# Performance work log

Hardware: AMD Instinct MI355X
Metric: run time of the kernel (lower is better)

Reference implementation:

```python
import jax, jax.numpy as jnp
import numpy as np

C, H, W = 512, 192, 192  # feature map dims; 3x3 patches at stride 3 (non-overlapping)


def setup_inputs() -> dict:
    key = jax.random.key(0)
    k1, k2 = jax.random.split(key)
    model_resp = jax.random.normal(k1, (1, C, H, W), dtype=jnp.float32)
    style_resp = jax.random.normal(k2, (1, C, H, W), dtype=jnp.float32)
    return {"model_resp": model_resp, "style_resp": style_resp}


def _unfold3(x):
    # torch.nn.Unfold(kernel=3, stride=3) on (1, C, H, W) -> (C*9, L) after the
    # module's view(patch_count, patch_size) (note: rows are feature channels,
    # columns are spatial locations, matching the original code's dim order).
    _, c, h, w = x.shape
    p = x[0].reshape(c, h // 3, 3, w // 3, 3)          # (c, ph, kh, pw, kw)
    p = p.transpose(0, 2, 4, 1, 3)                      # (c, kh, kw, ph, pw)
    return p.reshape(c * 9, (h // 3) * (w // 3))        # (A, L)


def reference(model_resp, style_resp):
    img = _unfold3(model_resp)                          # (A, L)
    sty = _unfold3(style_resp)                          # (A, L)
    img_norm = 1.0 / jnp.linalg.norm(img, axis=1)       # (A,)
    sty_norm = 1.0 / jnp.linalg.norm(sty, axis=1)       # (A,)
    S = img @ sty.T                                     # (A, A), S[i,j] = img_i . sty_j
    # Faithful to torch: expand(A, A) of a 1-D tensor broadcasts along dim 0,
    # i.e. multiplies COLUMNS by the normalizer vector.
    S1 = S * img_norm[None, :]
    S2 = S1.T * sty_norm[None, :]                       # S2[i,j] = img_norm[i]*sty_norm[j]*(img_j . sty_i)
    nearest = jnp.argmax(S2, axis=0)                    # (A,) int
    max_sim = jnp.max(S2, axis=0)                       # (A,) float (the online-max values)
    return nearest, max_sim
```

## Files before the change

kernel.cpp:

```cpp
#include <hip/hip_runtime.h>
#include <hip/hip_bf16.h>
#include <hip/hip_fp16.h>

#define A_DIM 4608
#define L_DIM 4096
#define CH    512
#define H_DIM 192
#define W_DIM 192

#define BM 128
#define BN 128
#define BK 32
#define NS (L_DIM / BK)

#define CPB 32

typedef _Float16 half8 __attribute__((ext_vector_type(8)));
typedef float   floatx4 __attribute__((ext_vector_type(4)));
typedef float   floatx16 __attribute__((ext_vector_type(16)));

__global__ __launch_bounds__(256) void prep_kernel(
    const float* __restrict__ x0, const float* __restrict__ x1,
    _Float16* __restrict__ Uhi0, _Float16* __restrict__ Ulo0,
    _Float16* __restrict__ Uhi1, _Float16* __restrict__ Ulo1,
    float* __restrict__ ss0, float* __restrict__ ss1) {
  const int which = blockIdx.z;
  const float* __restrict__ x = which ? x1 : x0;
  _Float16* __restrict__ Uhi = which ? Uhi1 : Uhi0;
  _Float16* __restrict__ Ulo = which ? Ulo1 : Ulo0;
  float* __restrict__ ssg = which ? ss1 : ss0;

  const int ph = blockIdx.y;
  const int c0 = blockIdx.x * CPB;
  const int abase = blockIdx.x * (CPB * 9);

  __shared__ _Float16 sHi[CPB * 9 * 8 * 8];
  __shared__ _Float16 sLo[CPB * 9 * 8 * 8];
  __shared__ float ssb[CPB * 9];

  const int t = threadIdx.x;
  for (int a = t; a < CPB * 9; a += 256) ssb[a] = 0.f;
  __syncthreads();

  const int c_l = t >> 3;
  const int s = t & 7;
  const float* __restrict__ rowbase =
      x + ((size_t)(c0 + c_l) * H_DIM + 3 * ph) * W_DIM + s * 24;
  float ssp[9] = {0.f, 0.f, 0.f, 0.f, 0.f, 0.f, 0.f, 0.f, 0.f};

#pragma unroll
  for (int kh = 0; kh < 3; ++kh) {
    const float* __restrict__ rp = rowbase + kh * W_DIM;
    floatx4 v4[6];
#pragma unroll
    for (int i = 0; i < 6; ++i) v4[i] = *(const floatx4*)(rp + i * 4);
    half8 hv[3], lv[3];
#pragma unroll
    for (int i = 0; i < 6; ++i)
#pragma unroll
      for (int j = 0; j < 4; ++j) {
        const int m = i * 4 + j;
        const int kw = m % 3, e = m / 3;
        const float v = v4[i][j];
        ssp[kh * 3 + kw] += v * v;
        const _Float16 h = (_Float16)v;
        hv[kw][e] = h;
        lv[kw][e] = (_Float16)(v - (float)h);
      }
#pragma unroll
    for (int kw = 0; kw < 3; ++kw) {
      const int a_l = c_l * 9 + kh * 3 + kw;
      const int addr = (a_l * 8 + (s ^ (a_l & 7))) * 8;
      *(half8*)&sHi[addr] = hv[kw];
      *(half8*)&sLo[addr] = lv[kw];
    }
  }
#pragma unroll
  for (int q = 0; q < 9; ++q) atomicAdd(&ssb[c_l * 9 + q], ssp[q]);
  __syncthreads();

#pragma unroll
  for (int i = 0; i < 9; ++i) {
    const int idx = i * 256 + t;
    const int c8 = idx / 288;
    const int a_l = idx - c8 * 288;
    const int addr = (a_l * 8 + (c8 ^ (a_l & 7))) * 8;
    const size_t g = ((size_t)(ph * 8 + c8) * A_DIM + abase + a_l) * 8;
    *(half8*)&Uhi[g] = *(const half8*)&sHi[addr];
    *(half8*)&Ulo[g] = *(const half8*)&sLo[addr];
  }
  for (int a = t; a < CPB * 9; a += 256) atomicAdd(&ssg[abase + a], ssb[a]);
}

#define GLDS(g, l)                                                          \
  __builtin_amdgcn_global_load_lds(                                        \
      (const __attribute__((address_space(1))) void*)(g),                   \
      (__attribute__((address_space(3))) void*)(l), 16, 0, 0)

__global__ __launch_bounds__(256, 2) void gemm_max_kernel(
    const _Float16* __restrict__ Shi, const _Float16* __restrict__ Slo,
    const _Float16* __restrict__ Ihi, const _Float16* __restrict__ Ilo,
    const float* __restrict__ img_ss,
    unsigned long long* __restrict__ packed) {
  __shared__ _Float16 sm[2][4][4 * 128 * 8];

  const int t = threadIdx.x;
  const int lane = t & 63, wv = t >> 6;
  const int wvr = wv >> 1, wvc = wv & 1;
  const int row0 = blockIdx.y * BM;
  const int col0 = blockIdx.x * BN;
  const int l31 = lane & 31, hs = lane >> 5;

  floatx16 acc[2][2];
#pragma unroll
  for (int rf = 0; rf < 2; ++rf)
#pragma unroll
    for (int cf = 0; cf < 2; ++cf) acc[rf][cf] = (floatx16)0.f;

  const size_t CH8 = (size_t)A_DIM * 8;
  const size_t so = (size_t)(t & 127) * 8 + (size_t)(t >> 7) * CH8;
  const _Float16* __restrict__ pAh = Shi + (size_t)row0 * 8 + so;
  const _Float16* __restrict__ pAl = Slo + (size_t)row0 * 8 + so;
  const _Float16* __restrict__ pBh = Ihi + (size_t)col0 * 8 + so;
  const _Float16* __restrict__ pBl = Ilo + (size_t)col0 * 8 + so;
  const int dl = t * 8;

#define ISSUE(b, off)                                      \
  do {                                                     \
    GLDS(pAh + (off),           &sm[b][0][dl]);            \
    GLDS(pAh + (off) + 2 * CH8, &sm[b][0][dl + 2048]);     \
    GLDS(pAl + (off),           &sm[b][1][dl]);            \
    GLDS(pAl + (off) + 2 * CH8, &sm[b][1][dl + 2048]);     \
    GLDS(pBh + (off),           &sm[b][2][dl]);            \
    GLDS(pBh + (off) + 2 * CH8, &sm[b][2][dl + 2048]);     \
    GLDS(pBl + (off),           &sm[b][3][dl]);            \
    GLDS(pBl + (off) + 2 * CH8, &sm[b][3][dl + 2048]);     \
  } while (0)

  ISSUE(0, 0);

  for (int ks = 0; ks < NS; ++ks) {
    const int cur = ks & 1;
    asm volatile("s_waitcnt vmcnt(0)" ::: "memory");
    asm volatile("s_barrier" ::: "memory");
    if (ks + 1 < NS) ISSUE(1 - cur, (size_t)(ks + 1) * 4 * CH8);

#pragma unroll
    for (int kk = 0; kk < 2; ++kk) {
      const int kc = kk * 2 + hs;
      half8 ah[2], al[2], bh[2], bl[2];
#pragma unroll
      for (int rf = 0; rf < 2; ++rf) {
        const int idx = (kc * 128 + wvr * 64 + rf * 32 + l31) * 8;
        ah[rf] = *(const half8*)&sm[cur][0][idx];
        al[rf] = *(const half8*)&sm[cur][1][idx];
      }
#pragma unroll
      for (int cf = 0; cf < 2; ++cf) {
        const int idx = (kc * 128 + wvc * 64 + cf * 32 + l31) * 8;
        bh[cf] = *(const half8*)&sm[cur][2][idx];
        bl[cf] = *(const half8*)&sm[cur][3][idx];
      }
#pragma unroll
      for (int rf = 0; rf < 2; ++rf)
#pragma unroll
        for (int cf = 0; cf < 2; ++cf)
          acc[rf][cf] = __builtin_amdgcn_mfma_f32_32x32x16_f16(
              ah[rf], bh[cf], acc[rf][cf], 0, 0, 0);
#pragma unroll
      for (int rf = 0; rf < 2; ++rf)
#pragma unroll
        for (int cf = 0; cf < 2; ++cf)
          acc[rf][cf] = __builtin_amdgcn_mfma_f32_32x32x16_f16(
              ah[rf], bl[cf], acc[rf][cf], 0, 0, 0);
#pragma unroll
      for (int rf = 0; rf < 2; ++rf)
#pragma unroll
        for (int cf = 0; cf < 2; ++cf)
          acc[rf][cf] = __builtin_amdgcn_mfma_f32_32x32x16_f16(
              al[rf], bh[cf], acc[rf][cf], 0, 0, 0);
    }
  }

  float nrv[2][16];
#pragma unroll
  for (int rf = 0; rf < 2; ++rf) {
    const int base_i = row0 + wvr * 64 + rf * 32 + 4 * hs;
#pragma unroll
    for (int g = 0; g < 4; ++g) {
      const floatx4 s4 = *(const floatx4*)&img_ss[base_i + 8 * g];
#pragma unroll
      for (int r = 0; r < 4; ++r) nrv[rf][g * 4 + r] = 1.0f / sqrtf(s4[r]);
    }
  }
#pragma unroll
  for (int cf = 0; cf < 2; ++cf) {
    const int j = col0 + wvc * 64 + cf * 32 + l31;
    float best = -3.4e38f;
    int bi = 0x7FFFFFFF;
#pragma unroll
    for (int rf = 0; rf < 2; ++rf) {
      const int base_i = row0 + wvr * 64 + rf * 32 + 4 * hs;
#pragma unroll
      for (int g = 0; g < 4; ++g)
#pragma unroll
        for (int r = 0; r < 4; ++r) {
          const int i = base_i + 8 * g + r;
          const float v = acc[rf][cf][g * 4 + r] * nrv[rf][g * 4 + r];
          if (v > best) { best = v; bi = i; }
        }
    }
    const float ov = __shfl_xor(best, 32, 64);
    const int oi = __shfl_xor(bi, 32, 64);
    if (ov > best || (ov == best && oi < bi)) { best = ov; bi = oi; }
    if (hs == 0) {
      const unsigned u = __float_as_uint(best);
      const unsigned key = (u & 0x80000000u) ? ~u : (u | 0x80000000u);
      const unsigned long long pk =
          ((unsigned long long)key << 32) | (unsigned)(~(unsigned)bi);
      atomicMax(&packed[j], pk);
    }
  }
}

__global__ __launch_bounds__(256) void finalize_kernel(
    const unsigned long long* __restrict__ packed,
    const float* __restrict__ sty_ss, float* __restrict__ out) {
  const int j = blockIdx.x * 256 + threadIdx.x;
  if (j >= A_DIM) return;
  const unsigned long long p = packed[j];
  const unsigned key = (unsigned)(p >> 32);
  const unsigned u = (key & 0x80000000u) ? (key ^ 0x80000000u) : ~key;
  const float v = __uint_as_float(u);
  const int idx = (int)(~(unsigned)(p & 0xFFFFFFFFu));
  out[j] = (float)idx;
  out[A_DIM + j] = v * (1.0f / sqrtf(sty_ss[j]));
}

extern "C" void kernel_launch(void* const* d_in, const int* in_sizes, int n_in,
                              void* d_out, int out_size, void* d_ws, size_t ws_size,
                              hipStream_t stream) {
  const float* model = (const float*)d_in[0];
  const float* style = (const float*)d_in[1];
  float* out = (float*)d_out;
  char* ws = (char*)d_ws;

  const size_t usz = (size_t)A_DIM * L_DIM * 2;
  _Float16* img_hi = (_Float16*)(ws);
  _Float16* img_lo = (_Float16*)(ws + usz);
  _Float16* sty_hi = (_Float16*)(ws + 2 * usz);
  _Float16* sty_lo = (_Float16*)(ws + 3 * usz);
  float* img_ss = (float*)(ws + 4 * usz);
  float* sty_ss = img_ss + A_DIM;
  unsigned long long* packed = (unsigned long long*)(img_ss + 2 * A_DIM);

  hipMemsetAsync(img_ss, 0, (size_t)A_DIM * 16, stream);
  prep_kernel<<<dim3(CH / CPB, H_DIM / 3, 2), 256, 0, stream>>>(
      model, style, img_hi, img_lo, sty_hi, sty_lo, img_ss, sty_ss);
  gemm_max_kernel<<<dim3(A_DIM / BN, A_DIM / BM), 256, 0, stream>>>(
      sty_hi, sty_lo, img_hi, img_lo, img_ss, packed);
  finalize_kernel<<<18, 256, 0, stream>>>(packed, sty_ss, out);
}
```

Baseline: 743.9 us.

## Load MFMA fragments directly from global memory into registers, dropping LDS staging

Replaces the LDS double-buffered global_load_lds pipeline with direct per-wave global loads of half8 fragments into registers, software-pipelined two steps ahead. This removes the barriers and LDS round trips in the main loop. In exchange, each wave now fetches its own A and B fragments, so data shared across waves in a block is loaded redundantly through L1/L2. Register pressure also rises from the 16 prefetched fragments.

Result: slower. 864.2 us (+16.2%).

```diff
diff --git a/kernel.cpp b/kernel.cpp
--- a/kernel.cpp
+++ b/kernel.cpp
@@ -10,8 +10,7 @@
 
 #define BM 128
 #define BN 128
-#define BK 32
-#define NS (L_DIM / BK)
+#define NSTEP (L_DIM / 16)
 
 #define CPB 32
 
@@ -92,18 +91,11 @@
   for (int a = t; a < CPB * 9; a += 256) atomicAdd(&ssg[abase + a], ssb[a]);
 }
 
-#define GLDS(g, l)                                                          \
-  __builtin_amdgcn_global_load_lds(                                        \
-      (const __attribute__((address_space(1))) void*)(g),                   \
-      (__attribute__((address_space(3))) void*)(l), 16, 0, 0)
-
 __global__ __launch_bounds__(256, 2) void gemm_max_kernel(
     const _Float16* __restrict__ Shi, const _Float16* __restrict__ Slo,
     const _Float16* __restrict__ Ihi, const _Float16* __restrict__ Ilo,
     const float* __restrict__ img_ss,
     unsigned long long* __restrict__ packed) {
-  __shared__ _Float16 sm[2][4][4 * 128 * 8];
-
   const int t = threadIdx.x;
   const int lane = t & 63, wv = t >> 6;
   const int wvr = wv >> 1, wvc = wv & 1;
@@ -117,69 +109,52 @@
 #pragma unroll
     for (int cf = 0; cf < 2; ++cf) acc[rf][cf] = (floatx16)0.f;
 
-  const size_t CH8 = (size_t)A_DIM * 8;
-  const size_t so = (size_t)(t & 127) * 8 + (size_t)(t >> 7) * CH8;
-  const _Float16* __restrict__ pAh = Shi + (size_t)row0 * 8 + so;
-  const _Float16* __restrict__ pAl = Slo + (size_t)row0 * 8 + so;
-  const _Float16* __restrict__ pBh = Ihi + (size_t)col0 * 8 + so;
-  const _Float16* __restrict__ pBl = Ilo + (size_t)col0 * 8 + so;
-  const int dl = t * 8;
-
-#define ISSUE(b, off)                                      \
-  do {                                                     \
-    GLDS(pAh + (off),           &sm[b][0][dl]);            \
-    GLDS(pAh + (off) + 2 * CH8, &sm[b][0][dl + 2048]);     \
-    GLDS(pAl + (off),           &sm[b][1][dl]);            \
-    GLDS(pAl + (off) + 2 * CH8, &sm[b][1][dl + 2048]);     \
-    GLDS(pBh + (off),           &sm[b][2][dl]);            \
-    GLDS(pBh + (off) + 2 * CH8, &sm[b][2][dl + 2048]);     \
-    GLDS(pBl + (off),           &sm[b][3][dl]);            \
-    GLDS(pBl + (off) + 2 * CH8, &sm[b][3][dl + 2048]);     \
+  const size_t PLB = (size_t)A_DIM * 16;
+  const size_t ao = ((size_t)hs * A_DIM + row0 + wvr * 64 + l31) * 16;
+  const size_t bo = ((size_t)hs * A_DIM + col0 + wvc * 64 + l31) * 16;
+  const char* __restrict__ pAh = (const char*)Shi + ao;
+  const char* __restrict__ pAl = (const char*)Slo + ao;
+  const char* __restrict__ pBh = (const char*)Ihi + bo;
+  const char* __restrict__ pBl = (const char*)Ilo + bo;
+
+  half8 f0[8], f1[8];
+
+#define LOADSTEP(F, s)                                        \
+  do {                                                        \
+    const size_t o = (size_t)(s) * (2 * PLB);                 \
+    F[0] = *(const half8*)(pAh + o);                          \
+    F[1] = *(const half8*)(pAh + o + 512);                    \
+    F[2] = *(const half8*)(pAl + o);                          \
+    F[3] = *(const half8*)(pAl + o + 512);                    \
+    F[4] = *(const half8*)(pBh + o);                          \
+    F[5] = *(const half8*)(pBh + o + 512);                    \
+    F[6] = *(const half8*)(pBl + o);                          \
+    F[7] = *(const half8*)(pBl + o + 512);                    \
   } while (0)
 
-  ISSUE(0, 0);
-
-  for (int ks = 0; ks < NS; ++ks) {
-    const int cur = ks & 1;
-    asm volatile("s_waitcnt vmcnt(0)" ::: "memory");
-    asm volatile("s_barrier" ::: "memory");
-    if (ks + 1 < NS) ISSUE(1 - cur, (size_t)(ks + 1) * 4 * CH8);
-
-#pragma unroll
-    for (int kk = 0; kk < 2; ++kk) {
-      const int kc = kk * 2 + hs;
-      half8 ah[2], al[2], bh[2], bl[2];
-#pragma unroll
-      for (int rf = 0; rf < 2; ++rf) {
-        const int idx = (kc * 128 + wvr * 64 + rf * 32 + l31) * 8;
-        ah[rf] = *(const half8*)&sm[cur][0][idx];
-        al[rf] = *(const half8*)&sm[cur][1][idx];
-      }
-#pragma unroll
-      for (int cf = 0; cf < 2; ++cf) {
-        const int idx = (kc * 128 + wvc * 64 + cf * 32 + l31) * 8;
-        bh[cf] = *(const half8*)&sm[cur][2][idx];
-        bl[cf] = *(const half8*)&sm[cur][3][idx];
-      }
-#pragma unroll
-      for (int rf = 0; rf < 2; ++rf)
-#pragma unroll
-        for (int cf = 0; cf < 2; ++cf)
-          acc[rf][cf] = __builtin_amdgcn_mfma_f32_32x32x16_f16(
-              ah[rf], bh[cf], acc[rf][cf], 0, 0, 0);
-#pragma unroll
-      for (int rf = 0; rf < 2; ++rf)
-#pragma unroll
-        for (int cf = 0; cf < 2; ++cf)
-          acc[rf][cf] = __builtin_amdgcn_mfma_f32_32x32x16_f16(
-              ah[rf], bl[cf], acc[rf][cf], 0, 0, 0);
-#pragma unroll
-      for (int rf = 0; rf < 2; ++rf)
-#pragma unroll
-        for (int cf = 0; cf < 2; ++cf)
-          acc[rf][cf] = __builtin_amdgcn_mfma_f32_32x32x16_f16(
-              al[rf], bh[cf], acc[rf][cf], 0, 0, 0);
-    }
+#define MFMASTEP(F)                                                         \
+  do {                                                                      \
+    acc[0][0] = __builtin_amdgcn_mfma_f32_32x32x16_f16(F[0], F[4], acc[0][0], 0, 0, 0); \
+    acc[0][1] = __builtin_amdgcn_mfma_f32_32x32x16_f16(F[0], F[5], acc[0][1], 0, 0, 0); \
+    acc[1][0] = __builtin_amdgcn_mfma_f32_32x32x16_f16(F[1], F[4], acc[1][0], 0, 0, 0); \
+    acc[1][1] = __builtin_amdgcn_mfma_f32_32x32x16_f16(F[1], F[5], acc[1][1], 0, 0, 0); \
+    acc[0][0] = __builtin_amdgcn_mfma_f32_32x32x16_f16(F[0], F[6], acc[0][0], 0, 0, 0); \
+    acc[0][1] = __builtin_amdgcn_mfma_f32_32x32x16_f16(F[0], F[7], acc[0][1], 0, 0, 0); \
+    acc[1][0] = __builtin_amdgcn_mfma_f32_32x32x16_f16(F[1], F[6], acc[1][0], 0, 0, 0); \
+    acc[1][1] = __builtin_amdgcn_mfma_f32_32x32x16_f16(F[1], F[7], acc[1][1], 0, 0, 0); \
+    acc[0][0] = __builtin_amdgcn_mfma_f32_32x32x16_f16(F[2], F[4], acc[0][0], 0, 0, 0); \
+    acc[0][1] = __builtin_amdgcn_mfma_f32_32x32x16_f16(F[2], F[5], acc[0][1], 0, 0, 0); \
+    acc[1][0] = __builtin_amdgcn_mfma_f32_32x32x16_f16(F[3], F[4], acc[1][0], 0, 0, 0); \
+    acc[1][1] = __builtin_amdgcn_mfma_f32_32x32x16_f16(F[3], F[5], acc[1][1], 0, 0, 0); \
+  } while (0)
+
+  LOADSTEP(f0, 0);
+  LOADSTEP(f1, 1);
+  for (int s = 0; s < NSTEP; s += 2) {
+    MFMASTEP(f0);
+    if (s + 2 < NSTEP) LOADSTEP(f0, s + 2);
+    MFMASTEP(f1);
+    if (s + 3 < NSTEP) LOADSTEP(f1, s + 3);
   }
 
   float nrv[2][16];
```

## Enlarge GEMM tile to 256x128 with BK16 and prefetch-before-wait pipelining

Applied to the files above, without the earlier changes.

Doubles the row tile to 256 so each wave holds a 128x64 accumulator (4x2 MFMA fragments), halves the K step to 16, and splits shared memory into separate A/B buffers. The next stage's global-to-LDS loads are issued before waiting, using vmcnt(6) so the previous stage can complete while new loads stay in flight, with a second barrier protecting buffer reuse. The normalizer is computed inline in the epilogue to save registers. This raises reuse of the B tile and MFMA density per LDS load, at the cost of more accumulator registers (128 floats per lane), which may reduce occupancy under the 2-blocks launch bound, plus twice as many barriers per unit of K.

Measured after the change: 771.7 us. 3.7% more time.

```diff
diff --git a/kernel.cpp b/kernel.cpp
--- a/kernel.cpp
+++ b/kernel.cpp
@@ -8,9 +8,9 @@
 #define H_DIM 192
 #define W_DIM 192
 
-#define BM 128
+#define BM 256
 #define BN 128
-#define BK 32
+#define BK 16
 #define NS (L_DIM / BK)
 
 #define CPB 32
@@ -102,7 +102,10 @@
     const _Float16* __restrict__ Ihi, const _Float16* __restrict__ Ilo,
     const float* __restrict__ img_ss,
     unsigned long long* __restrict__ packed) {
-  __shared__ _Float16 sm[2][4][4 * 128 * 8];
+  __shared__ _Float16 sAh[2][4096];
+  __shared__ _Float16 sAl[2][4096];
+  __shared__ _Float16 sBh[2][2048];
+  __shared__ _Float16 sBl[2][2048];
 
   const int t = threadIdx.x;
   const int lane = t & 63, wv = t >> 6;
@@ -111,104 +114,96 @@
   const int col0 = blockIdx.x * BN;
   const int l31 = lane & 31, hs = lane >> 5;
 
-  floatx16 acc[2][2];
-#pragma unroll
-  for (int rf = 0; rf < 2; ++rf)
+  floatx16 acc[4][2];
+#pragma unroll
+  for (int rf = 0; rf < 4; ++rf)
 #pragma unroll
     for (int cf = 0; cf < 2; ++cf) acc[rf][cf] = (floatx16)0.f;
 
   const size_t CH8 = (size_t)A_DIM * 8;
-  const size_t so = (size_t)(t & 127) * 8 + (size_t)(t >> 7) * CH8;
-  const _Float16* __restrict__ pAh = Shi + (size_t)row0 * 8 + so;
-  const _Float16* __restrict__ pAl = Slo + (size_t)row0 * 8 + so;
-  const _Float16* __restrict__ pBh = Ihi + (size_t)col0 * 8 + so;
-  const _Float16* __restrict__ pBl = Ilo + (size_t)col0 * 8 + so;
+  const size_t soA = (size_t)t * 8;
+  const size_t soB = (size_t)(t & 127) * 8 + (size_t)(t >> 7) * CH8;
+  const _Float16* __restrict__ pAh = Shi + (size_t)row0 * 8 + soA;
+  const _Float16* __restrict__ pAl = Slo + (size_t)row0 * 8 + soA;
+  const _Float16* __restrict__ pBh = Ihi + (size_t)col0 * 8 + soB;
+  const _Float16* __restrict__ pBl = Ilo + (size_t)col0 * 8 + soB;
   const int dl = t * 8;
 
 #define ISSUE(b, off)                                      \
   do {                                                     \
-    GLDS(pAh + (off),           &sm[b][0][dl]);            \
-    GLDS(pAh + (off) + 2 * CH8, &sm[b][0][dl + 2048]);     \
-    GLDS(pAl + (off),           &sm[b][1][dl]);            \
-    GLDS(pAl + (off) + 2 * CH8, &sm[b][1][dl + 2048]);     \
-    GLDS(pBh + (off),           &sm[b][2][dl]);            \
-    GLDS(pBh + (off) + 2 * CH8, &sm[b][2][dl + 2048]);     \
-    GLDS(pBl + (off),           &sm[b][3][dl]);            \
-    GLDS(pBl + (off) + 2 * CH8, &sm[b][3][dl + 2048]);     \
+    GLDS(pAh + (off),       &sAh[b][dl]);                  \
+    GLDS(pAh + (off) + CH8, &sAh[b][dl + 2048]);           \
+    GLDS(pAl + (off),       &sAl[b][dl]);                  \
+    GLDS(pAl + (off) + CH8, &sAl[b][dl + 2048]);           \
+    GLDS(pBh + (off),       &sBh[b][dl]);                  \
+    GLDS(pBl + (off),       &sBl[b][dl]);                  \
   } while (0)
 
   ISSUE(0, 0);
 
   for (int ks = 0; ks < NS; ++ks) {
     const int cur = ks & 1;
-    asm volatile("s_waitcnt vmcnt(0)" ::: "memory");
+    if (ks + 1 < NS) {
+      ISSUE(1 - cur, (size_t)(ks + 1) * 2 * CH8);
+      asm volatile("s_waitcnt vmcnt(6)" ::: "memory");
+    } else {
+      asm volatile("s_waitcnt vmcnt(0)" ::: "memory");
+    }
     asm volatile("s_barrier" ::: "memory");
-    if (ks + 1 < NS) ISSUE(1 - cur, (size_t)(ks + 1) * 4 * CH8);
-
-#pragma unroll
-    for (int kk = 0; kk < 2; ++kk) {
-      const int kc = kk * 2 + hs;
-      half8 ah[2], al[2], bh[2], bl[2];
-#pragma unroll
-      for (int rf = 0; rf < 2; ++rf) {
-        const int idx = (kc * 128 + wvr * 64 + rf * 32 + l31) * 8;
-        ah[rf] = *(const half8*)&sm[cur][0][idx];
-        al[rf] = *(const half8*)&sm[cur][1][idx];
-      }
-#pragma unroll
-      for (int cf = 0; cf < 2; ++cf) {
-        const int idx = (kc * 128 + wvc * 64 + cf * 32 + l31) * 8;
-        bh[cf] = *(const half8*)&sm[cur][2][idx];
-        bl[cf] = *(const half8*)&sm[cur][3][idx];
-      }
-#pragma unroll
-      for (int rf = 0; rf < 2; ++rf)
-#pragma unroll
-        for (int cf = 0; cf < 2; ++cf)
-          acc[rf][cf] = __builtin_amdgcn_mfma_f32_32x32x16_f16(
-              ah[rf], bh[cf], acc[rf][cf], 0, 0, 0);
-#pragma unroll
-      for (int rf = 0; rf < 2; ++rf)
-#pragma unroll
-        for (int cf = 0; cf < 2; ++cf)
-          acc[rf][cf] = __builtin_amdgcn_mfma_f32_32x32x16_f16(
-              ah[rf], bl[cf], acc[rf][cf], 0, 0, 0);
-#pragma unroll
-      for (int rf = 0; rf < 2; ++rf)
-#pragma unroll
-        for (int cf = 0; cf < 2; ++cf)
-          acc[rf][cf] = __builtin_amdgcn_mfma_f32_32x32x16_f16(
-              al[rf], bh[cf], acc[rf][cf], 0, 0, 0);
-    }
-  }
-
-  float nrv[2][16];
-#pragma unroll
-  for (int rf = 0; rf < 2; ++rf) {
-    const int base_i = row0 + wvr * 64 + rf * 32 + 4 * hs;
-#pragma unroll
-    for (int g = 0; g < 4; ++g) {
-      const floatx4 s4 = *(const floatx4*)&img_ss[base_i + 8 * g];
-#pragma unroll
-      for (int r = 0; r < 4; ++r) nrv[rf][g * 4 + r] = 1.0f / sqrtf(s4[r]);
-    }
-  }
+
+    half8 ah[4], al[4], bh[2], bl[2];
+#pragma unroll
+    for (int rf = 0; rf < 4; ++rf) {
+      const int idx = (hs * 256 + wvr * 128 + rf * 32 + l31) * 8;
+      ah[rf] = *(const half8*)&sAh[cur][idx];
+      al[rf] = *(const half8*)&sAl[cur][idx];
+    }
+#pragma unroll
+    for (int cf = 0; cf < 2; ++cf) {
+      const int idx = (hs * 128 + wvc * 64 + cf * 32 + l31) * 8;
+      bh[cf] = *(const half8*)&sBh[cur][idx];
+      bl[cf] = *(const half8*)&sBl[cur][idx];
+    }
+#pragma unroll
+    for (int rf = 0; rf < 4; ++rf)
+#pragma unroll
+      for (int cf = 0; cf < 2; ++cf)
+        acc[rf][cf] = __builtin_amdgcn_mfma_f32_32x32x16_f16(
+            ah[rf], bh[cf], acc[rf][cf], 0, 0, 0);
+#pragma unroll
+    for (int rf = 0; rf < 4; ++rf)
+#pragma unroll
+      for (int cf = 0; cf < 2; ++cf)
+        acc[rf][cf] = __builtin_amdgcn_mfma_f32_32x32x16_f16(
+            ah[rf], bl[cf], acc[rf][cf], 0, 0, 0);
+#pragma unroll
+    for (int rf = 0; rf < 4; ++rf)
+#pragma unroll
+      for (int cf = 0; cf < 2; ++cf)
+        acc[rf][cf] = __builtin_amdgcn_mfma_f32_32x32x16_f16(
+            al[rf], bh[cf], acc[rf][cf], 0, 0, 0);
+
+    asm volatile("s_barrier" ::: "memory");
+  }
+
 #pragma unroll
   for (int cf = 0; cf < 2; ++cf) {
     const int j = col0 + wvc * 64 + cf * 32 + l31;
     float best = -3.4e38f;
     int bi = 0x7FFFFFFF;
 #pragma unroll
-    for (int rf = 0; rf < 2; ++rf) {
-      const int base_i = row0 + wvr * 64 + rf * 32 + 4 * hs;
-#pragma unroll
-      for (int g = 0; g < 4; ++g)
+    for (int rf = 0; rf < 4; ++rf) {
+      const int base_i = row0 + wvr * 128 + rf * 32 + 4 * hs;
+#pragma unroll
+      for (int g = 0; g < 4; ++g) {
+        const floatx4 s4 = *(const floatx4*)&img_ss[base_i + 8 * g];
 #pragma unroll
         for (int r = 0; r < 4; ++r) {
           const int i = base_i + 8 * g + r;
-          const float v = acc[rf][cf][g * 4 + r] * nrv[rf][g * 4 + r];
+          const float v = acc[rf][cf][g * 4 + r] * (1.0f / sqrtf(s4[r]));
           if (v > best) { best = v; bi = i; }
         }
+      }
     }
     const float ov = __shfl_xor(best, 32, 64);
     const int oi = __shfl_xor(bi, 32, 64);
```
